# Kernel tuning notes

Measured on AMD Instinct MI355X. Metric: run time of the kernel, lower is better.

## Reference

```python
import jax, jax.numpy as jnp
import numpy as np

N_NODES = 20000
N_EDGES = 320000
D = 512
N_LAYERS = 3
LN_EPS = 1e-5


def setup_inputs() -> dict:
    key = jax.random.key(0)
    k0, k1, k2, k3 = jax.random.split(key, 4)
    feats = jax.random.normal(k0, (N_NODES, D), dtype=jnp.float32)
    src = jax.random.randint(k1, (N_EDGES,), 0, N_NODES)
    dst = jax.random.randint(k2, (N_EDGES,), 0, N_NODES)
    ln_g = jnp.ones((N_LAYERS, D), dtype=jnp.float32)
    ln_b = jnp.zeros((N_LAYERS, D), dtype=jnp.float32)
    # Glorot-ish init for GraphConv weights [L, in, out]
    W = jax.random.normal(k3, (N_LAYERS, D, D), dtype=jnp.float32) * (1.0 / np.sqrt(D)).astype(np.float32)
    b = jnp.zeros((N_LAYERS, D), dtype=jnp.float32)
    return {"feats": feats, "src": src, "dst": dst, "ln_g": ln_g, "ln_b": ln_b, "W": W, "b": b}


def reference(feats, src, dst, ln_g, ln_b, W, b):
    n = feats.shape[0]
    ones_e = jnp.ones(src.shape[0], dtype=feats.dtype)
    # symmetric 'both' normalization, degrees clamped to >=1 (allow_zero_in_degree)
    out_deg = jnp.maximum(jax.ops.segment_sum(ones_e, src, num_segments=n), 1.0)
    in_deg = jnp.maximum(jax.ops.segment_sum(ones_e, dst, num_segments=n), 1.0)
    norm_src = jax.lax.rsqrt(out_deg)[:, None]  # [N,1]
    norm_dst = jax.lax.rsqrt(in_deg)[:, None]   # [N,1]

    h = feats
    L = W.shape[0]
    for i in range(L):
        # LayerNorm
        mu = jnp.mean(h, axis=-1, keepdims=True)
        var = jnp.mean(jnp.square(h - mu), axis=-1, keepdims=True)
        h = (h - mu) * jax.lax.rsqrt(var + LN_EPS) * ln_g[i] + ln_b[i]
        # GraphConv norm='both': D_in^{-1/2} A D_out^{-1/2} (X W) + b
        h = (h * norm_src) @ W[i]            # [N,D] (weight-first; linear, order-equivalent)
        msg = h[src]                         # [E,D] gather
        agg = jax.ops.segment_sum(msg, dst, num_segments=n)  # [N,D] scatter-add
        h = agg * norm_dst + b[i]
        if i < L - 1:
            h = jax.nn.relu(h)  # dropout is identity in eval mode
    return h
```

## Files before the change

kernel.cpp:

```cpp
#include <hip/hip_runtime.h>
#include <hip/hip_bf16.h>
#include <stdint.h>

#define DIMD 512
#define LNEPS 1e-5f

typedef __attribute__((ext_vector_type(8))) short short8;
typedef __attribute__((ext_vector_type(4))) float f32x4;

static __device__ __forceinline__ unsigned short f2bf(float x) {
  unsigned u = __builtin_bit_cast(unsigned, x);
  unsigned r = (u + 0x7FFFu + ((u >> 16) & 1u)) >> 16;
  return (unsigned short)r;
}
static __device__ __forceinline__ float bf2f(unsigned short h) {
  return __builtin_bit_cast(float, ((unsigned)h) << 16);
}


__global__ __launch_bounds__(256) void deg_kernel(const int* __restrict__ src, const int* __restrict__ dst,
                                                  int* __restrict__ outdeg, int* __restrict__ indeg, int e) {
  int i = blockIdx.x * 256 + threadIdx.x;
  if (i < e) {
    atomicAdd(&outdeg[src[i]], 1);
    atomicAdd(&indeg[dst[i]], 1);
  }
}

__global__ __launch_bounds__(256) void norm_kernel(const int* __restrict__ outdeg, const int* __restrict__ indeg,
                                                   float* __restrict__ ns, float* __restrict__ nd, int n) {
  int i = blockIdx.x * 256 + threadIdx.x;
  if (i < n) {
    ns[i] = rsqrtf((float)max(outdeg[i], 1));
    nd[i] = rsqrtf((float)max(indeg[i], 1));
  }
}

__global__ __launch_bounds__(1024) void scan_kernel(const int* __restrict__ cnt, int* __restrict__ rp,
                                                    int* __restrict__ cursor, int n) {
  __shared__ int wsum[16];
  __shared__ int carry_s;
  const int tid = threadIdx.x;
  const int lane = tid & 63;
  const int wid = tid >> 6;
  if (tid == 0) carry_s = 0;
  __syncthreads();
  for (int base = 0; base < n; base += 1024) {
    const int i = base + tid;
    const int x = (i < n) ? cnt[i] : 0;
    int incl = x;
    #pragma unroll
    for (int o = 1; o < 64; o <<= 1) {
      int t = __shfl_up(incl, o);
      if (lane >= o) incl += t;
    }
    if (lane == 63) wsum[wid] = incl;
    __syncthreads();
    if (wid == 0) {
      int v = (lane < 16) ? wsum[lane] : 0;
      #pragma unroll
      for (int o = 1; o < 16; o <<= 1) {
        int t = __shfl_up(v, o);
        if (lane >= o) v += t;
      }
      if (lane < 16) wsum[lane] = v;
    }
    __syncthreads();
    const int carry = carry_s;
    const int woff = wid ? wsum[wid - 1] : 0;
    if (i < n) {
      const int excl = carry + woff + incl - x;
      rp[i] = excl;
      cursor[i] = excl;
    }
    __syncthreads();
    if (tid == 0) carry_s = carry + wsum[15];
    __syncthreads();
  }
  if (tid == 0) rp[n] = carry_s;
}

__global__ __launch_bounds__(256) void fill_kernel(const int* __restrict__ src, const int* __restrict__ dst,
                                                   int* __restrict__ cursor, int* __restrict__ eidx, int e) {
  int i = blockIdx.x * 256 + threadIdx.x;
  if (i < e) {
    int p = atomicAdd(&cursor[dst[i]], 1);
    eidx[p] = src[i];
  }
}


__global__ __launch_bounds__(256) void wsplit_kernel(const float* __restrict__ W,
                                                     unsigned short* __restrict__ WhiT, int total) {
  int idx = blockIdx.x * 256 + threadIdx.x;
  if (idx >= total) return;
  int l = idx >> 18;
  int rem = idx & 262143;
  int k = rem >> 9;
  int nn = rem & 511;
  float w = W[idx];
  size_t o = ((size_t)l << 18) + ((size_t)nn << 9) + (size_t)k;
  WhiT[o] = f2bf(w);
}


__global__ __launch_bounds__(128) void ln_split_kernel(const float* __restrict__ h,
                                                       unsigned short* __restrict__ Abf,
                                                       const float* __restrict__ g, const float* __restrict__ bb,
                                                       const float* __restrict__ ns) {
  int v = blockIdx.x;
  int tid = threadIdx.x;
  const float4* hv = (const float4*)(h + (size_t)v * DIMD);
  float4 x = hv[tid];
  float s = x.x + x.y + x.z + x.w;
  #pragma unroll
  for (int m = 32; m; m >>= 1) s += __shfl_xor(s, m);
  __shared__ float red[2];
  __shared__ float red2[2];
  int wid = tid >> 6;
  if ((tid & 63) == 0) red[wid] = s;
  __syncthreads();
  float mu = (red[0] + red[1]) * (1.0f / 512.0f);
  float4 c = make_float4(x.x - mu, x.y - mu, x.z - mu, x.w - mu);
  float s2 = c.x * c.x + c.y * c.y + c.z * c.z + c.w * c.w;
  #pragma unroll
  for (int m = 32; m; m >>= 1) s2 += __shfl_xor(s2, m);
  if ((tid & 63) == 0) red2[wid] = s2;
  __syncthreads();
  float var = (red2[0] + red2[1]) * (1.0f / 512.0f);
  float rstd = rsqrtf(var + LNEPS);
  float scale = ns[v];
  float4 g4 = ((const float4*)g)[tid];
  float4 b4 = ((const float4*)bb)[tid];
  ushort4 h4;
  h4.x = f2bf((c.x * rstd * g4.x + b4.x) * scale);
  h4.y = f2bf((c.y * rstd * g4.y + b4.y) * scale);
  h4.z = f2bf((c.z * rstd * g4.z + b4.z) * scale);
  h4.w = f2bf((c.w * rstd * g4.w + b4.w) * scale);
  ((ushort4*)(Abf + (size_t)v * DIMD))[tid] = h4;
}


__global__ __launch_bounds__(128) void ln_scale_kernel(const float* __restrict__ h, float* __restrict__ out,
                                                       const float* __restrict__ g, const float* __restrict__ bb,
                                                       const float* __restrict__ ns) {
  int v = blockIdx.x;
  int tid = threadIdx.x;
  const float4* hv = (const float4*)(h + (size_t)v * DIMD);
  float4 x = hv[tid];
  float s = x.x + x.y + x.z + x.w;
  #pragma unroll
  for (int m = 32; m; m >>= 1) s += __shfl_xor(s, m);
  __shared__ float red[2];
  __shared__ float red2[2];
  int wid = tid >> 6;
  if ((tid & 63) == 0) red[wid] = s;
  __syncthreads();
  float mu = (red[0] + red[1]) * (1.0f / 512.0f);
  float4 c = make_float4(x.x - mu, x.y - mu, x.z - mu, x.w - mu);
  float s2 = c.x * c.x + c.y * c.y + c.z * c.z + c.w * c.w;
  #pragma unroll
  for (int m = 32; m; m >>= 1) s2 += __shfl_xor(s2, m);
  if ((tid & 63) == 0) red2[wid] = s2;
  __syncthreads();
  float var = (red2[0] + red2[1]) * (1.0f / 512.0f);
  float rstd = rsqrtf(var + LNEPS);
  float scale = ns[v];
  float4 g4 = ((const float4*)g)[tid];
  float4 b4 = ((const float4*)bb)[tid];
  float4 o;
  o.x = (c.x * rstd * g4.x + b4.x) * scale;
  o.y = (c.y * rstd * g4.y + b4.y) * scale;
  o.z = (c.z * rstd * g4.z + b4.z) * scale;
  o.w = (c.w * rstd * g4.w + b4.w) * scale;
  ((float4*)(out + (size_t)v * DIMD))[tid] = o;
}


__global__ __launch_bounds__(256, 4) void gemm_mfma_bf16out(const unsigned short* __restrict__ Abf,
                                                            const unsigned short* __restrict__ BhiT,
                                                            unsigned short* __restrict__ C, int M) {
  __shared__ char lds[16384];
  char* sA = lds;
  char* sB = lds + 8192;
  const int tid = threadIdx.x;
  const int lane = tid & 63;
  const int w = tid >> 6;
  const int tileM = blockIdx.y * 128;
  const int tileN = blockIdx.x * 128;
  const int wm = (w >> 1) * 64;
  const int wn = (w & 1) * 64;

  f32x4 acc[4][4] = {};

  for (int k0 = 0; k0 < DIMD; k0 += 32) {
    #pragma unroll
    for (int i = 0; i < 2; ++i) {
      const int c = i * 256 + tid;
      const int r = c >> 2;
      const int q = c & 3;
      const int kb = (q ^ ((r >> 1) & 3)) * 16;
      int gra = tileM + r; gra = gra < M ? gra : M - 1;
      const size_t aoff = (size_t)gra * (DIMD * 2) + (size_t)(k0 * 2 + kb);
      const size_t boff = (size_t)(tileN + r) * (DIMD * 2) + (size_t)(k0 * 2 + kb);
      const int lbase = c * 16;
      __builtin_amdgcn_global_load_lds((const __attribute__((address_space(1))) unsigned int*)((const char*)Abf + aoff),
                                       (__attribute__((address_space(3))) unsigned int*)(sA + lbase), 16, 0, 0);
      __builtin_amdgcn_global_load_lds((const __attribute__((address_space(1))) unsigned int*)((const char*)BhiT + boff),
                                       (__attribute__((address_space(3))) unsigned int*)(sB + lbase), 16, 0, 0);
    }
    __syncthreads();
    const int qr = lane >> 4;
    short8 ah[4], bh[4];
    #pragma unroll
    for (int mf = 0; mf < 4; ++mf) {
      const int r = wm + mf * 16 + (lane & 15);
      const int kb = (qr ^ ((r >> 1) & 3)) * 16;
      ah[mf] = *(const short8*)(sA + r * 64 + kb);
    }
    #pragma unroll
    for (int nf = 0; nf < 4; ++nf) {
      const int r = wn + nf * 16 + (lane & 15);
      const int kb = (qr ^ ((r >> 1) & 3)) * 16;
      bh[nf] = *(const short8*)(sB + r * 64 + kb);
    }
    #pragma unroll
    for (int mf = 0; mf < 4; ++mf) {
      #pragma unroll
      for (int nf = 0; nf < 4; ++nf) {
        acc[mf][nf] = __builtin_amdgcn_mfma_f32_16x16x32_bf16(ah[mf], bh[nf], acc[mf][nf], 0, 0, 0);
      }
    }
    __syncthreads();
  }
  #pragma unroll
  for (int mf = 0; mf < 4; ++mf) {
    const int rb = tileM + wm + mf * 16 + (lane >> 4) * 4;
    #pragma unroll
    for (int nf = 0; nf < 4; ++nf) {
      const int col = tileN + wn + nf * 16 + (lane & 15);
      #pragma unroll
      for (int j = 0; j < 4; ++j) {
        const int row = rb + j;
        if (row < M) C[(size_t)row * DIMD + col] = f2bf(acc[mf][nf][j]);
      }
    }
  }
}


__global__ __launch_bounds__(256) void gemm_fp32(const float* __restrict__ A, const float* __restrict__ W,
                                                 float* __restrict__ C, int M) {
  const int K = DIMD, N = DIMD;
  __shared__ float As[16][65];
  __shared__ float Bs[16][64];
  int tid = threadIdx.x;
  int tileM = blockIdx.x * 64;
  int tileN = blockIdx.y * 64;
  int tx = tid & 15, ty = tid >> 4;
  float acc[4][4] = {};
  int arow = tid >> 2;
  int acol = (tid & 3) * 4;
  int brow = tid >> 4;
  int bcol = (tid & 15) * 4;

  for (int k0 = 0; k0 < K; k0 += 16) {
    float4 a4 = make_float4(0.f, 0.f, 0.f, 0.f);
    int gr = tileM + arow;
    if (gr < M) a4 = *(const float4*)(A + (size_t)gr * K + k0 + acol);
    As[acol + 0][arow] = a4.x;
    As[acol + 1][arow] = a4.y;
    As[acol + 2][arow] = a4.z;
    As[acol + 3][arow] = a4.w;
    float4 b4 = *(const float4*)(W + (size_t)(k0 + brow) * N + tileN + bcol);
    *(float4*)(&Bs[brow][bcol]) = b4;
    __syncthreads();
    #pragma unroll
    for (int kk = 0; kk < 16; ++kk) {
      float a[4];
      #pragma unroll
      for (int i = 0; i < 4; ++i) a[i] = As[kk][ty * 4 + i];
      float4 b = *(const float4*)(&Bs[kk][tx * 4]);
      #pragma unroll
      for (int i = 0; i < 4; ++i) {
        acc[i][0] += a[i] * b.x;
        acc[i][1] += a[i] * b.y;
        acc[i][2] += a[i] * b.z;
        acc[i][3] += a[i] * b.w;
      }
    }
    __syncthreads();
  }
  #pragma unroll
  for (int i = 0; i < 4; ++i) {
    int gr = tileM + ty * 4 + i;
    if (gr < M) {
      float4 o = make_float4(acc[i][0], acc[i][1], acc[i][2], acc[i][3]);
      *(float4*)(C + (size_t)gr * N + tileN + tx * 4) = o;
    }
  }
}


template <int MODE>
__global__ __launch_bounds__(256) void agg_fused(const unsigned short* __restrict__ Y,
                                                 const int* __restrict__ rp, const int* __restrict__ eidx,
                                                 const float* __restrict__ nd, const float* __restrict__ bias,
                                                 const float* __restrict__ g, const float* __restrict__ bb,
                                                 const float* __restrict__ ns,
                                                 unsigned short* __restrict__ Abf,
                                                 float* __restrict__ outf, int n) {
  const int lane = threadIdx.x & 63;
  const int v = blockIdx.x * 4 + (threadIdx.x >> 6);
  if (v >= n) return;
  const int beg = rp[v], end = rp[v + 1];
  float acc[8] = {0.f, 0.f, 0.f, 0.f, 0.f, 0.f, 0.f, 0.f};
  int j = beg;
  for (; j + 7 < end; j += 8) {
    const short8 m0 = *(const short8*)(Y + (size_t)eidx[j] * DIMD + lane * 8);
    const short8 m1 = *(const short8*)(Y + (size_t)eidx[j + 1] * DIMD + lane * 8);
    const short8 m2 = *(const short8*)(Y + (size_t)eidx[j + 2] * DIMD + lane * 8);
    const short8 m3 = *(const short8*)(Y + (size_t)eidx[j + 3] * DIMD + lane * 8);
    const short8 m4 = *(const short8*)(Y + (size_t)eidx[j + 4] * DIMD + lane * 8);
    const short8 m5 = *(const short8*)(Y + (size_t)eidx[j + 5] * DIMD + lane * 8);
    const short8 m6 = *(const short8*)(Y + (size_t)eidx[j + 6] * DIMD + lane * 8);
    const short8 m7 = *(const short8*)(Y + (size_t)eidx[j + 7] * DIMD + lane * 8);
    #pragma unroll
    for (int k = 0; k < 8; ++k)
      acc[k] += ((bf2f((unsigned short)m0[k]) + bf2f((unsigned short)m1[k])) +
                 (bf2f((unsigned short)m2[k]) + bf2f((unsigned short)m3[k]))) +
                ((bf2f((unsigned short)m4[k]) + bf2f((unsigned short)m5[k])) +
                 (bf2f((unsigned short)m6[k]) + bf2f((unsigned short)m7[k])));
  }
  for (; j + 3 < end; j += 4) {
    const short8 m0 = *(const short8*)(Y + (size_t)eidx[j] * DIMD + lane * 8);
    const short8 m1 = *(const short8*)(Y + (size_t)eidx[j + 1] * DIMD + lane * 8);
    const short8 m2 = *(const short8*)(Y + (size_t)eidx[j + 2] * DIMD + lane * 8);
    const short8 m3 = *(const short8*)(Y + (size_t)eidx[j + 3] * DIMD + lane * 8);
    #pragma unroll
    for (int k = 0; k < 8; ++k)
      acc[k] += (bf2f((unsigned short)m0[k]) + bf2f((unsigned short)m1[k])) +
                (bf2f((unsigned short)m2[k]) + bf2f((unsigned short)m3[k]));
  }
  for (; j < end; ++j) {
    const short8 m0 = *(const short8*)(Y + (size_t)eidx[j] * DIMD + lane * 8);
    #pragma unroll
    for (int k = 0; k < 8; ++k) acc[k] += bf2f((unsigned short)m0[k]);
  }
  const float f = nd[v];
  const float4 bA = ((const float4*)(bias))[lane * 2];
  const float4 bB = ((const float4*)(bias))[lane * 2 + 1];
  float o[8];
  o[0] = acc[0] * f + bA.x; o[1] = acc[1] * f + bA.y; o[2] = acc[2] * f + bA.z; o[3] = acc[3] * f + bA.w;
  o[4] = acc[4] * f + bB.x; o[5] = acc[5] * f + bB.y; o[6] = acc[6] * f + bB.z; o[7] = acc[7] * f + bB.w;
  if (MODE == 0) {
    #pragma unroll
    for (int k = 0; k < 8; ++k) o[k] = fmaxf(o[k], 0.f);
    float s = 0.f;
    #pragma unroll
    for (int k = 0; k < 8; ++k) s += o[k];
    #pragma unroll
    for (int m = 32; m; m >>= 1) s += __shfl_xor(s, m);
    const float mu = s * (1.0f / 512.0f);
    float s2 = 0.f;
    float c[8];
    #pragma unroll
    for (int k = 0; k < 8; ++k) { c[k] = o[k] - mu; s2 += c[k] * c[k]; }
    #pragma unroll
    for (int m = 32; m; m >>= 1) s2 += __shfl_xor(s2, m);
    const float rstd = rsqrtf(s2 * (1.0f / 512.0f) + LNEPS);
    const float scale = ns[v];
    const float4 gA = ((const float4*)(g))[lane * 2];
    const float4 gB = ((const float4*)(g))[lane * 2 + 1];
    const float4 lA = ((const float4*)(bb))[lane * 2];
    const float4 lB = ((const float4*)(bb))[lane * 2 + 1];
    short8 hv;
    hv[0] = (short)f2bf((c[0] * rstd * gA.x + lA.x) * scale);
    hv[1] = (short)f2bf((c[1] * rstd * gA.y + lA.y) * scale);
    hv[2] = (short)f2bf((c[2] * rstd * gA.z + lA.z) * scale);
    hv[3] = (short)f2bf((c[3] * rstd * gA.w + lA.w) * scale);
    hv[4] = (short)f2bf((c[4] * rstd * gB.x + lB.x) * scale);
    hv[5] = (short)f2bf((c[5] * rstd * gB.y + lB.y) * scale);
    hv[6] = (short)f2bf((c[6] * rstd * gB.z + lB.z) * scale);
    hv[7] = (short)f2bf((c[7] * rstd * gB.w + lB.w) * scale);
    *(short8*)(Abf + (size_t)v * DIMD + lane * 8) = hv;
  } else {
    float4 oA = make_float4(o[0], o[1], o[2], o[3]);
    float4 oB = make_float4(o[4], o[5], o[6], o[7]);
    ((float4*)(outf + (size_t)v * DIMD + lane * 8))[0] = oA;
    ((float4*)(outf + (size_t)v * DIMD + lane * 8))[1] = oB;
  }
}


__global__ __launch_bounds__(128) void agg_kernel(const float* __restrict__ Y, const int* __restrict__ rp,
                                                  const int* __restrict__ eidx, const float* __restrict__ nd,
                                                  const float* __restrict__ bias, float* __restrict__ out,
                                                  int do_relu) {
  int v = blockIdx.x;
  int tid = threadIdx.x;
  int beg = rp[v], end = rp[v + 1];
  float4 acc = make_float4(0.f, 0.f, 0.f, 0.f);
  for (int j = beg; j < end; ++j) {
    int s = eidx[j];
    float4 m = ((const float4*)(Y + (size_t)s * DIMD))[tid];
    acc.x += m.x; acc.y += m.y; acc.z += m.z; acc.w += m.w;
  }
  float f = nd[v];
  float4 b4 = ((const float4*)bias)[tid];
  float4 o = make_float4(acc.x * f + b4.x, acc.y * f + b4.y, acc.z * f + b4.z, acc.w * f + b4.w);
  if (do_relu) {
    o.x = fmaxf(o.x, 0.f); o.y = fmaxf(o.y, 0.f); o.z = fmaxf(o.z, 0.f); o.w = fmaxf(o.w, 0.f);
  }
  ((float4*)(out + (size_t)v * DIMD))[tid] = o;
}


extern "C" void kernel_launch(void* const* d_in, const int* in_sizes, int n_in,
                              void* d_out, int out_size, void* d_ws, size_t ws_size,
                              hipStream_t stream) {
  const float* feats = (const float*)d_in[0];
  const int* src = (const int*)d_in[1];
  const int* dst = (const int*)d_in[2];
  const float* ln_g = (const float*)d_in[3];
  const float* ln_b = (const float*)d_in[4];
  const float* W = (const float*)d_in[5];
  const float* bias = (const float*)d_in[6];
  const int n = in_sizes[0] / DIMD;
  const int e = in_sizes[1];
  const int L = in_sizes[3] / DIMD;

  char* ws = (char*)d_ws;
  size_t off = 0;
  auto alloc = [&](size_t bytes) {
    void* p = ws + off;
    off = (off + bytes + 255) & ~(size_t)255;
    return p;
  };

  const size_t misc_bytes = ((size_t)n * 4 + 256) * 6 + ((size_t)(n + 1) * 4 + 256) + ((size_t)e * 4 + 256);
  const size_t fast_need = ((size_t)(n + 128) * DIMD * 2 + 256)
                         + ((size_t)n * DIMD * 2 + 256)
                         + ((size_t)L * DIMD * DIMD * 2 + 256)
                         + misc_bytes;

  const bool fast = ws_size >= fast_need;

  float* O = (float*)d_out;
  int eb = (e + 255) / 256;
  int nb = (n + 255) / 256;

  if (fast) {
    unsigned short* Abf = (unsigned short*)alloc((size_t)(n + 128) * DIMD * 2);
    unsigned short* Ybf = (unsigned short*)alloc((size_t)n * DIMD * 2);
    unsigned short* WhiT = (unsigned short*)alloc((size_t)L * DIMD * DIMD * 2);
    float* ns = (float*)alloc((size_t)n * 4);
    float* nd = (float*)alloc((size_t)n * 4);
    int* outdeg = (int*)alloc((size_t)n * 4);
    int* indeg = (int*)alloc((size_t)n * 4);
    int* rp = (int*)alloc((size_t)(n + 1) * 4);
    int* cursor = (int*)alloc((size_t)n * 4);
    int* eidx = (int*)alloc((size_t)e * 4);

    hipMemsetAsync(outdeg, 0, (size_t)n * 4, stream);
    hipMemsetAsync(indeg, 0, (size_t)n * 4, stream);

    int wtot = L * DIMD * DIMD;
    wsplit_kernel<<<(wtot + 255) / 256, 256, 0, stream>>>(W, WhiT, wtot);
    deg_kernel<<<eb, 256, 0, stream>>>(src, dst, outdeg, indeg, e);
    norm_kernel<<<nb, 256, 0, stream>>>(outdeg, indeg, ns, nd, n);
    scan_kernel<<<1, 1024, 0, stream>>>(indeg, rp, cursor, n);
    fill_kernel<<<eb, 256, 0, stream>>>(src, dst, cursor, eidx, e);

    dim3 ggrid(DIMD / 128, (n + 127) / 128);
    int agrid = (n + 3) / 4;
    ln_split_kernel<<<n, 128, 0, stream>>>(feats, Abf, ln_g, ln_b, ns);
    for (int l = 0; l < L; ++l) {
      gemm_mfma_bf16out<<<ggrid, 256, 0, stream>>>(Abf, WhiT + (size_t)l * DIMD * DIMD, Ybf, n);
      if (l < L - 1) {
        agg_fused<0><<<agrid, 256, 0, stream>>>(Ybf, rp, eidx, nd, bias + (size_t)l * DIMD,
                                                ln_g + (size_t)(l + 1) * DIMD, ln_b + (size_t)(l + 1) * DIMD,
                                                ns, Abf, nullptr, n);
      } else {
        agg_fused<1><<<agrid, 256, 0, stream>>>(Ybf, rp, eidx, nd, bias + (size_t)l * DIMD,
                                                nullptr, nullptr, nullptr, nullptr, O, n);
      }
    }
  } else {
    float* X = (float*)alloc((size_t)n * DIMD * 4);
    float* ns = (float*)alloc((size_t)n * 4);
    float* nd = (float*)alloc((size_t)n * 4);
    int* outdeg = (int*)alloc((size_t)n * 4);
    int* indeg = (int*)alloc((size_t)n * 4);
    int* rp = (int*)alloc((size_t)(n + 1) * 4);
    int* cursor = (int*)alloc((size_t)n * 4);
    int* eidx = (int*)alloc((size_t)e * 4);

    hipMemsetAsync(outdeg, 0, (size_t)n * 4, stream);
    hipMemsetAsync(indeg, 0, (size_t)n * 4, stream);

    deg_kernel<<<eb, 256, 0, stream>>>(src, dst, outdeg, indeg, e);
    norm_kernel<<<nb, 256, 0, stream>>>(outdeg, indeg, ns, nd, n);
    scan_kernel<<<1, 1024, 0, stream>>>(indeg, rp, cursor, n);
    fill_kernel<<<eb, 256, 0, stream>>>(src, dst, cursor, eidx, e);

    const float* cur = feats;
    dim3 ggrid((n + 63) / 64, DIMD / 64);
    for (int l = 0; l < L; ++l) {
      int s = 3 * l;
      float* ln_out = (s & 1) ? X : O;
      float* mm_out = ((s + 1) & 1) ? X : O;
      float* ag_out = ((s + 2) & 1) ? X : O;
      ln_scale_kernel<<<n, 128, 0, stream>>>(cur, ln_out, ln_g + (size_t)l * DIMD, ln_b + (size_t)l * DIMD, ns);
      gemm_fp32<<<ggrid, 256, 0, stream>>>(ln_out, W + (size_t)l * DIMD * DIMD, mm_out, n);
      agg_kernel<<<n, 128, 0, stream>>>(mm_out, rp, eidx, nd, bias + (size_t)l * DIMD, ag_out, (l < L - 1) ? 1 : 0);
      cur = ag_out;
    }
  }
}
```

Measured before the change: 296.0 us.

## Double-buffer LDS in bf16 MFMA GEMM to overlap global loads with compute

```diff
diff --git a/kernel.cpp b/kernel.cpp
--- a/kernel.cpp
+++ b/kernel.cpp
@@ -180,9 +180,7 @@
 __global__ __launch_bounds__(256, 4) void gemm_mfma_bf16out(const unsigned short* __restrict__ Abf,
                                                             const unsigned short* __restrict__ BhiT,
                                                             unsigned short* __restrict__ C, int M) {
-  __shared__ char lds[16384];
-  char* sA = lds;
-  char* sB = lds + 8192;
+  __shared__ char lds[32768];
   const int tid = threadIdx.x;
   const int lane = tid & 63;
   const int w = tid >> 6;
@@ -193,7 +191,9 @@
 
   f32x4 acc[4][4] = {};
 
-  for (int k0 = 0; k0 < DIMD; k0 += 32) {
+  auto stage = [&](int buf, int k0) {
+    char* sA = lds + buf * 16384;
+    char* sB = sA + 8192;
     #pragma unroll
     for (int i = 0; i < 2; ++i) {
       const int c = i * 256 + tid;
@@ -209,7 +209,11 @@
       __builtin_amdgcn_global_load_lds((const __attribute__((address_space(1))) unsigned int*)((const char*)BhiT + boff),
                                        (__attribute__((address_space(3))) unsigned int*)(sB + lbase), 16, 0, 0);
     }
-    __syncthreads();
+  };
+
+  auto compute = [&](int buf) {
+    char* sA = lds + buf * 16384;
+    char* sB = sA + 8192;
     const int qr = lane >> 4;
     short8 ah[4], bh[4];
     #pragma unroll
@@ -231,8 +235,28 @@
         acc[mf][nf] = __builtin_amdgcn_mfma_f32_16x16x32_bf16(ah[mf], bh[nf], acc[mf][nf], 0, 0, 0);
       }
     }
-    __syncthreads();
-  }
+  };
+
+  stage(0, 0);
+  int cur = 0;
+  #pragma unroll 1
+  for (int ks = 0; ks < (DIMD / 32) - 1; ++ks) {
+    stage(cur ^ 1, (ks + 1) * 32);
+    __builtin_amdgcn_sched_barrier(0);
+    asm volatile("s_waitcnt vmcnt(4)");
+    __builtin_amdgcn_s_barrier();
+    __builtin_amdgcn_sched_barrier(0);
+    compute(cur);
+    asm volatile("s_waitcnt lgkmcnt(0)");
+    __builtin_amdgcn_sched_barrier(0);
+    __builtin_amdgcn_s_barrier();
+    cur ^= 1;
+  }
+  asm volatile("s_waitcnt vmcnt(0)");
+  __builtin_amdgcn_s_barrier();
+  __builtin_amdgcn_sched_barrier(0);
+  compute(cur);
+
   #pragma unroll
   for (int mf = 0; mf < 4; ++mf) {
     const int rb = tileM + wm + mf * 16 + (lane >> 4) * 4;
```

Result: no change. 297.0 us (+0.3%).
